# Kernel tuning notes

Hardware: AMD Instinct MI355X
Metric: run time of the kernel (lower is better)

## Reference

```python
import jax, jax.numpy as jnp
import numpy as np

EPS = 1e-5
_INV_STD = 1.0 / np.sqrt(1.0 + EPS)  # eval-mode BN with running_mean=0, running_var=1


def conv1x1(x, w):
    # x: (B,C,H,W), w: (O,C) -> (B,O,H,W)
    return jnp.einsum('bchw,oc->bohw', x, w)


def bn_relu(x, gamma, beta):
    y = x * (_INV_STD * gamma)[None, :, None, None] + beta[None, :, None, None]
    return jax.nn.relu(y)


def setup_inputs() -> dict:
    key = jax.random.key(0)
    ks = jax.random.split(key, 8)
    B, C, H, W, Kc, Kp = 8, 512, 128, 128, 256, 19
    s = 0.02
    return {
        'x': jax.random.normal(ks[0], (B, C, H, W), jnp.float32),
        'proxy_feats': jax.random.normal(ks[1], (B, C, Kp, 1), jnp.float32),
        'wq1': jax.random.normal(ks[2], (Kc, C), jnp.float32) * s,
        'gq1': jnp.ones((Kc,), jnp.float32), 'bq1': jnp.zeros((Kc,), jnp.float32),
        'wq2': jax.random.normal(ks[3], (Kc, Kc), jnp.float32) * s,
        'gq2': jnp.ones((Kc,), jnp.float32), 'bq2': jnp.zeros((Kc,), jnp.float32),
        'wk1': jax.random.normal(ks[4], (Kc, C), jnp.float32) * s,
        'gk1': jnp.ones((Kc,), jnp.float32), 'bk1': jnp.zeros((Kc,), jnp.float32),
        'wk2': jax.random.normal(ks[5], (Kc, Kc), jnp.float32) * s,
        'gk2': jnp.ones((Kc,), jnp.float32), 'bk2': jnp.zeros((Kc,), jnp.float32),
        'wv': jax.random.normal(ks[6], (Kc, C), jnp.float32) * s,
        'gv': jnp.ones((Kc,), jnp.float32), 'bv': jnp.zeros((Kc,), jnp.float32),
        'wo': jax.random.normal(ks[7], (C, Kc), jnp.float32) * s,
        'go': jnp.ones((C,), jnp.float32), 'bo': jnp.zeros((C,), jnp.float32),
    }


def reference(x, proxy_feats, wq1, gq1, bq1, wq2, gq2, bq2,
              wk1, gk1, bk1, wk2, gk2, bk2, wv, gv, bv, wo, go, bo):
    B, C, H, W = x.shape
    Kc = wq1.shape[0]
    # projections: 1x1 conv -> BN(eval) -> ReLU chains
    q = bn_relu(conv1x1(bn_relu(conv1x1(x, wq1), gq1, bq1), wq2), gq2, bq2)          # (B,Kc,H,W)
    k = bn_relu(conv1x1(bn_relu(conv1x1(proxy_feats, wk1), gk1, bk1), wk2), gk2, bk2)[..., 0]  # (B,Kc,Kp)
    v = bn_relu(conv1x1(proxy_feats, wv), gv, bv)[..., 0]                             # (B,Kc,Kp)
    qf = q.reshape(B, Kc, H * W).transpose(0, 2, 1)                                   # (B,HW,Kc)
    sim = jnp.einsum('bnc,bck->bnk', qf, k) * (Kc ** -0.5)                            # (B,HW,Kp)
    att = jax.nn.softmax(sim, axis=-1)
    ctx = jnp.einsum('bnk,bck->bnc', att, v)                                          # (B,HW,Kc)
    ctx = ctx.transpose(0, 2, 1).reshape(B, Kc, H, W)
    return bn_relu(conv1x1(ctx, wo), go, bo)                                          # (B,C,H,W)
```

## Files before the change

kernel.cpp:

```cpp
#include <hip/hip_runtime.h>

#define INV_STD 0.9999950000374997f

typedef unsigned short u16;
typedef __bf16 bf16x8 __attribute__((ext_vector_type(8)));
typedef __bf16 bf16x4 __attribute__((ext_vector_type(4)));
typedef float f32x4 __attribute__((ext_vector_type(4)));

__device__ __forceinline__ u16 f2bf(float f) {
    unsigned int u = __float_as_uint(f);
    u += 0x7fffu + ((u >> 16) & 1u);
    return (u16)(u >> 16);
}

__device__ __forceinline__ void gl_lds16(const void* g, void* l) {
    __builtin_amdgcn_global_load_lds(
        (const __attribute__((address_space(1))) unsigned int*)(unsigned long long)g,
        (__attribute__((address_space(3))) unsigned int*)(unsigned int)(unsigned long long)l,
        16, 0, 0);
}

__device__ __forceinline__ f32x4 mfma16(bf16x8 a, bf16x8 b, f32x4 c) {
    return __builtin_amdgcn_mfma_f32_16x16x32_bf16(a, b, c, 0, 0, 0);
}

__device__ __forceinline__ unsigned lds_off(const void* p) {
    return (unsigned)(unsigned long long)p;
}

__device__ __forceinline__ bf16x4 tr_read(unsigned addr) {
    bf16x4 r;
    asm volatile("ds_read_b64_tr_b16 %0, %1" : "=v"(r) : "v"(addr));
    return r;
}

__device__ __forceinline__ bf16x8 ldg8(const u16* p) {
    return *(const bf16x8*)p;
}

__global__ void wprep(const float* __restrict__ wq1, const float* __restrict__ gq1,
                      const float* __restrict__ wq2, const float* __restrict__ gq2,
                      u16* __restrict__ WQ1B, u16* __restrict__ WQ2B) {
    int blk = blockIdx.x;
    int t = threadIdx.x;
    if (blk < 512) {
        long i = (long)blk * 256 + t;
        int o = (int)(i >> 9);
        int q = (int)(i & 511);
        int r = q & 31;
        int src = (q & ~31) + ((r >> 3) & 3) * 4 + (r & 3) + ((r >> 2) & 1) * 16;
        WQ1B[i] = f2bf(wq1[(long)o * 512 + src] * (INV_STD * gq1[o]));
    } else {
        long i = (long)(blk - 512) * 256 + t;
        int o = (int)(i >> 8);
        WQ2B[i] = f2bf(wq2[i] * (INV_STD * gq2[o]));
    }
}

__global__ __launch_bounds__(256) void kv_kernel(
    const float* __restrict__ proxy,
    const float* __restrict__ wk1, const float* __restrict__ gk1, const float* __restrict__ bk1,
    const float* __restrict__ wk2, const float* __restrict__ gk2, const float* __restrict__ bk2,
    const float* __restrict__ wv,  const float* __restrict__ gv,  const float* __restrict__ bv,
    u16* __restrict__ KB,
    float* __restrict__ VF)
{
    int b = blockIdx.x >> 5, p = blockIdx.x & 31;
    int t = threadIdx.x;
    if (p >= 19) {
        KB[((long)b * 32 + p) * 256 + t] = 0;
        VF[((long)b * 256 + t) * 32 + p] = 0.f;
        return;
    }
    __shared__ float px[512];
    __shared__ float k1[256];
    for (int i = t; i < 512; i += 256) px[i] = proxy[((long)b * 512 + i) * 19 + p];
    __syncthreads();
    float aK = 0.f, aV = 0.f;
    const float4* wk1r = (const float4*)(wk1 + (long)t * 512);
    const float4* wvr  = (const float4*)(wv  + (long)t * 512);
    const float4* pxv  = (const float4*)px;
    #pragma unroll 4
    for (int c = 0; c < 128; ++c) {
        float4 pv = pxv[c];
        float4 k4 = wk1r[c];
        float4 v4 = wvr[c];
        aK += k4.x * pv.x + k4.y * pv.y + k4.z * pv.z + k4.w * pv.w;
        aV += v4.x * pv.x + v4.y * pv.y + v4.z * pv.z + v4.w * pv.w;
    }
    float k1v = fmaxf(aK * (INV_STD * gk1[t]) + bk1[t], 0.f);
    float vv  = fmaxf(aV * (INV_STD * gv[t])  + bv[t],  0.f);
    k1[t] = k1v;
    VF[((long)b * 256 + t) * 32 + p] = vv;
    __syncthreads();
    float a2 = 0.f;
    const float4* wk2r = (const float4*)(wk2 + (long)t * 256);
    const float4* k1v4 = (const float4*)k1;
    #pragma unroll 4
    for (int c = 0; c < 64; ++c) {
        float4 w4 = wk2r[c];
        float4 kk = k1v4[c];
        a2 += w4.x * kk.x + w4.y * kk.y + w4.z * kk.z + w4.w * kk.w;
    }
    KB[((long)b * 32 + p) * 256 + t] = f2bf(fmaxf(a2 * (INV_STD * gk2[t]) + bk2[t], 0.f));
}

__global__ __launch_bounds__(256) void wov_kernel(
    const float* __restrict__ wo,
    const float* __restrict__ go,
    const float* __restrict__ VF,
    u16* __restrict__ WoVB)
{
    int b = blockIdx.x >> 1, half = blockIdx.x & 1;
    __shared__ float vs[256 * 20];
    int t = threadIdx.x;
    #pragma unroll
    for (int p = 0; p < 19; ++p)
        vs[t * 20 + p] = VF[((long)b * 256 + t) * 32 + p];
    __syncthreads();
    int ch = half * 256 + t;
    float g = INV_STD * go[ch];
    const float* wr = wo + (long)ch * 256;
    float acc[19];
    #pragma unroll
    for (int p = 0; p < 19; ++p) acc[p] = 0.f;
    for (int c = 0; c < 256; ++c) {
        float wv = wr[c];
        #pragma unroll
        for (int p = 0; p < 19; ++p) acc[p] += wv * vs[c * 20 + p];
    }
    u16* dst = WoVB + ((long)b * 512 + ch) * 32;
    #pragma unroll
    for (int p = 0; p < 19; ++p) dst[p] = f2bf(g * acc[p]);
    #pragma unroll
    for (int p = 19; p < 32; ++p) dst[p] = 0;
}

__global__ __launch_bounds__(256, 2) void fused_all(
    const float* __restrict__ X,
    const u16* __restrict__ W1,
    const float* __restrict__ b1,
    const u16* __restrict__ W2,
    const float* __restrict__ b2,
    const u16* __restrict__ KB,
    const u16* __restrict__ WoVB,
    const float* __restrict__ obias,
    float* __restrict__ out)
{
    __shared__ __align__(16) u16 xs[64 * 64];
    __shared__ __align__(16) u16 lB[2][256 * 32];
    __shared__ __align__(16) u16 q12s[64 * 264];
    __shared__ __align__(16) u16 atts[64 * 40];
    int t = threadIdx.x, lane = t & 63, w = t >> 6;
    int l16 = lane & 15, hi = lane >> 4;
    long m0 = (long)blockIdx.x * 64;
    int b = (int)(m0 >> 14);
    int pixg = (int)(m0 & 16383);
    const float* xb = X + (long)b * 512 * 16384 + pixg;
    int ca = t >> 4;
    int aa = t & 15;
    int rW = lane >> 2;
    int cW = (lane & 3) << 3;
    unsigned trb = lds_off(&xs[hi * 64 + l16]);

    {
        f32x4 acc[4][4] = {};
        float4 xr0, xr1, xr2, xr3;
        {
            const float* p0 = xb + (long)ca * 16384 + aa * 4;
            xr0 = *(const float4*)(p0);
            xr1 = *(const float4*)(p0 + 16L * 16384);
            xr2 = *(const float4*)(p0 + 32L * 16384);
            xr3 = *(const float4*)(p0 + 48L * 16384);
        }
        #define STW(XR, P) { \
            int c = (P) * 16 + ca; \
            ushort4 u; u.x = f2bf(XR.x); u.y = f2bf(XR.y); u.z = f2bf(XR.z); u.w = f2bf(XR.w); \
            *(ushort4*)&xs[((aa >> 2) * 16 + (c >> 2)) * 64 + (c & 3) * 16 + (aa & 3) * 4] = u; }
        for (int kt = 0; kt < 8; ++kt) {
            int k0 = kt << 6;
            if (kt > 0) __syncthreads();
            STW(xr0, 0) STW(xr1, 1) STW(xr2, 2) STW(xr3, 3)
            __syncthreads();
            bf16x8 bb0[4], bb1[4];
            #pragma unroll
            for (int j = 0; j < 4; ++j) {
                const u16* wr = W1 + (long)(w * 64 + j * 16 + l16) * 512 + k0 + hi * 8;
                bb0[j] = ldg8(wr);
                bb1[j] = ldg8(wr + 32);
            }
            if (kt < 7) {
                const float* p0 = xb + (long)(k0 + 64 + ca) * 16384 + aa * 4;
                xr0 = *(const float4*)(p0);
                xr1 = *(const float4*)(p0 + 16L * 16384);
                xr2 = *(const float4*)(p0 + 32L * 16384);
                xr3 = *(const float4*)(p0 + 48L * 16384);
            }
            bf16x4 lo0[4], hh0[4], lo1[4], hh1[4];
            #pragma unroll
            for (int i = 0; i < 4; ++i) {
                unsigned a0 = trb + i * 2048;
                lo0[i] = tr_read(a0);
                hh0[i] = tr_read(a0 + 512);
            }
            #pragma unroll
            for (int i = 0; i < 4; ++i) {
                unsigned a0 = trb + i * 2048 + 1024;
                lo1[i] = tr_read(a0);
                hh1[i] = tr_read(a0 + 512);
            }
            asm volatile("s_waitcnt lgkmcnt(8)" ::: "memory");
            __builtin_amdgcn_sched_barrier(0);
            #pragma unroll
            for (int i = 0; i < 4; ++i) {
                bf16x8 a = __builtin_shufflevector(lo0[i], hh0[i], 0, 1, 2, 3, 4, 5, 6, 7);
                #pragma unroll
                for (int j = 0; j < 4; ++j)
                    acc[i][j] = mfma16(a, bb0[j], acc[i][j]);
            }
            asm volatile("s_waitcnt lgkmcnt(0)" ::: "memory");
            __builtin_amdgcn_sched_barrier(0);
            #pragma unroll
            for (int i = 0; i < 4; ++i) {
                bf16x8 a = __builtin_shufflevector(lo1[i], hh1[i], 0, 1, 2, 3, 4, 5, 6, 7);
                #pragma unroll
                for (int j = 0; j < 4; ++j)
                    acc[i][j] = mfma16(a, bb1[j], acc[i][j]);
            }
        }
        #undef STW
        #pragma unroll
        for (int j = 0; j < 4; ++j) {
            int q = w * 4 + j;
            gl_lds16(W2 + (long)(q * 16 + rW) * 256 + cW, &lB[0][q * 512]);
        }
        float bj[4];
        #pragma unroll
        for (int j = 0; j < 4; ++j) bj[j] = b1[w * 64 + j * 16 + l16];
        #pragma unroll
        for (int i = 0; i < 4; ++i)
            #pragma unroll
            for (int r = 0; r < 4; ++r) {
                int pix = i * 16 + hi * 4 + r;
                #pragma unroll
                for (int j = 0; j < 4; ++j) {
                    float v = acc[i][j][r] + bj[j];
                    q12s[pix * 264 + w * 64 + j * 16 + l16] = f2bf(fmaxf(v, 0.f));
                }
            }
    }
    __syncthreads();
    {
        f32x4 acc[4][4] = {};
        #pragma unroll
        for (int c = 0; c < 8; ++c) {
            int cur = c & 1;
            if (c < 7) {
                int k1 = (c + 1) << 5;
                #pragma unroll
                for (int j = 0; j < 4; ++j) {
                    int q = w * 4 + j;
                    gl_lds16(W2 + (long)(q * 16 + rW) * 256 + k1 + cW, &lB[cur ^ 1][q * 512]);
                }
            }
            bf16x8 a[4], bb[4];
            #pragma unroll
            for (int i = 0; i < 4; ++i)
                a[i] = *(const bf16x8*)&q12s[(i * 16 + l16) * 264 + (c << 5) + hi * 8];
            #pragma unroll
            for (int j = 0; j < 4; ++j)
                bb[j] = *(const bf16x8*)&lB[cur][(w * 64 + j * 16 + l16) * 32 + hi * 8];
            #pragma unroll
            for (int i = 0; i < 4; ++i)
                #pragma unroll
                for (int j = 0; j < 4; ++j)
                    acc[i][j] = mfma16(a[i], bb[j], acc[i][j]);
            __syncthreads();
        }
        float bj[4];
        #pragma unroll
        for (int j = 0; j < 4; ++j) bj[j] = b2[w * 64 + j * 16 + l16];
        #pragma unroll
        for (int i = 0; i < 4; ++i)
            #pragma unroll
            for (int r = 0; r < 4; ++r) {
                int pix = i * 16 + hi * 4 + r;
                #pragma unroll
                for (int j = 0; j < 4; ++j) {
                    float v = acc[i][j][r] + bj[j];
                    q12s[pix * 264 + w * 64 + j * 16 + l16] = f2bf(fmaxf(v, 0.f));
                }
            }
    }
    __syncthreads();
    {
        f32x4 s0 = {}, s1 = {};
        #pragma unroll
        for (int ks = 0; ks < 8; ++ks) {
            bf16x8 a = *(const bf16x8*)&q12s[(w * 16 + l16) * 264 + ks * 32 + hi * 8];
            bf16x8 b0 = ldg8(KB + ((long)b * 32 + l16) * 256 + ks * 32 + hi * 8);
            bf16x8 b1v = ldg8(KB + ((long)b * 32 + 16 + l16) * 256 + ks * 32 + hi * 8);
            s0 = mfma16(a, b0, s0);
            s1 = mfma16(a, b1v, s1);
        }
        const float scale = 0.0625f;
        #pragma unroll
        for (int r = 0; r < 4; ++r) {
            float v0 = s0[r] * scale;
            float v1 = s1[r] * scale;
            float mx = fmaxf(v0, v1);
            mx = fmaxf(mx, __shfl_xor(mx, 1));
            mx = fmaxf(mx, __shfl_xor(mx, 2));
            mx = fmaxf(mx, __shfl_xor(mx, 4));
            mx = fmaxf(mx, __shfl_xor(mx, 8));
            float e0 = __expf(v0 - mx);
            float e1 = (l16 < 3) ? __expf(v1 - mx) : 0.f;
            float s = e0 + e1;
            s += __shfl_xor(s, 1);
            s += __shfl_xor(s, 2);
            s += __shfl_xor(s, 4);
            s += __shfl_xor(s, 8);
            float inv = 1.f / s;
            int pix = w * 16 + hi * 4 + r;
            atts[pix * 40 + l16] = f2bf(e0 * inv);
            atts[pix * 40 + 16 + l16] = (l16 < 3) ? f2bf(e1 * inv) : (u16)0;
        }
    }
    __syncthreads();
    {
        bf16x8 av[4], bv[8];
        #pragma unroll
        for (int mf = 0; mf < 4; ++mf)
            av[mf] = *(const bf16x8*)&atts[(mf * 16 + l16) * 40 + hi * 8];
        #pragma unroll
        for (int nf = 0; nf < 8; ++nf)
            bv[nf] = ldg8(WoVB + ((long)b * 512 + w * 128 + nf * 16 + l16) * 32 + hi * 8);
        #pragma unroll
        for (int nf = 0; nf < 8; ++nf) {
            int ch = w * 128 + nf * 16 + l16;
            float bc = obias[ch];
            float* orow = out + ((long)b * 512 + ch) * 16384 + pixg;
            #pragma unroll
            for (int mf = 0; mf < 4; ++mf) {
                f32x4 acc = mfma16(av[mf], bv[nf], (f32x4){0.f, 0.f, 0.f, 0.f});
                float4 v;
                v.x = fmaxf(acc[0] + bc, 0.f);
                v.y = fmaxf(acc[1] + bc, 0.f);
                v.z = fmaxf(acc[2] + bc, 0.f);
                v.w = fmaxf(acc[3] + bc, 0.f);
                *(float4*)&orow[mf * 16 + hi * 4] = v;
            }
        }
    }
}

extern "C" void kernel_launch(void* const* d_in, const int* in_sizes, int n_in,
                              void* d_out, int out_size, void* d_ws, size_t ws_size,
                              hipStream_t stream) {
    const float* x    = (const float*)d_in[0];
    const float* prox = (const float*)d_in[1];
    const float* wq1  = (const float*)d_in[2];
    const float* gq1  = (const float*)d_in[3];
    const float* bq1  = (const float*)d_in[4];
    const float* wq2  = (const float*)d_in[5];
    const float* gq2  = (const float*)d_in[6];
    const float* bq2  = (const float*)d_in[7];
    const float* wk1  = (const float*)d_in[8];
    const float* gk1  = (const float*)d_in[9];
    const float* bk1  = (const float*)d_in[10];
    const float* wk2  = (const float*)d_in[11];
    const float* gk2  = (const float*)d_in[12];
    const float* bk2  = (const float*)d_in[13];
    const float* wv   = (const float*)d_in[14];
    const float* gv   = (const float*)d_in[15];
    const float* bv   = (const float*)d_in[16];
    const float* wo   = (const float*)d_in[17];
    const float* go   = (const float*)d_in[18];
    const float* bo   = (const float*)d_in[19];
    float* out = (float*)d_out;

    char* ws = (char*)d_ws;
    u16*   KB   = (u16*)(ws);
    float* VF   = (float*)(ws + 131072);
    u16*   WoVB = (u16*)(ws + 393216);
    u16*   WQ1B = (u16*)(ws + 655360);
    u16*   WQ2B = (u16*)(ws + 917504);

    wprep<<<768, 256, 0, stream>>>(wq1, gq1, wq2, gq2, WQ1B, WQ2B);
    kv_kernel<<<256, 256, 0, stream>>>(prox, wk1, gk1, bk1, wk2, gk2, bk2, wv, gv, bv, KB, VF);
    wov_kernel<<<16, 256, 0, stream>>>(wo, go, VF, WoVB);
    fused_all<<<2048, 256, 0, stream>>>(x, WQ1B, bq1, WQ2B, bq2, KB, WoVB, bo, out);
}
```

Measured before the change: 235.6 us.

## Load W2 fragments directly into registers instead of LDS double-buffering

The second GEMM (q1→q2) now loads its W2 B-operand fragments straight from global memory into registers, using a two-deep register prefetch with manual vmcnt waits, in place of the global_load_lds double buffer. This removes the 32KB lB LDS buffer and the per-iteration __syncthreads. With less LDS in use, launch bounds go from 2 to 3 blocks per SM for higher occupancy. The risks are register pressure under the tighter bound, which may cause spills, and exposed global-load latency, because W2 is now fetched per wave with no sharing through LDS.

Measured after the change: 268.7 us. 14.0% more time.

```diff
diff --git a/kernel.cpp b/kernel.cpp
--- a/kernel.cpp
+++ b/kernel.cpp
@@ -13,13 +13,6 @@
     return (u16)(u >> 16);
 }
 
-__device__ __forceinline__ void gl_lds16(const void* g, void* l) {
-    __builtin_amdgcn_global_load_lds(
-        (const __attribute__((address_space(1))) unsigned int*)(unsigned long long)g,
-        (__attribute__((address_space(3))) unsigned int*)(unsigned int)(unsigned long long)l,
-        16, 0, 0);
-}
-
 __device__ __forceinline__ f32x4 mfma16(bf16x8 a, bf16x8 b, f32x4 c) {
     return __builtin_amdgcn_mfma_f32_16x16x32_bf16(a, b, c, 0, 0, 0);
 }
@@ -36,6 +29,12 @@
 
 __device__ __forceinline__ bf16x8 ldg8(const u16* p) {
     return *(const bf16x8*)p;
+}
+
+__device__ __forceinline__ bf16x8 ldg8_asm(const u16* p) {
+    bf16x8 r;
+    asm volatile("global_load_dwordx4 %0, %1, off" : "=v"(r) : "v"(p));
+    return r;
 }
 
 __global__ void wprep(const float* __restrict__ wq1, const float* __restrict__ gq1,
@@ -136,7 +135,7 @@
     for (int p = 19; p < 32; ++p) dst[p] = 0;
 }
 
-__global__ __launch_bounds__(256, 2) void fused_all(
+__global__ __launch_bounds__(256, 3) void fused_all(
     const float* __restrict__ X,
     const u16* __restrict__ W1,
     const float* __restrict__ b1,
@@ -148,7 +147,6 @@
     float* __restrict__ out)
 {
     __shared__ __align__(16) u16 xs[64 * 64];
-    __shared__ __align__(16) u16 lB[2][256 * 32];
     __shared__ __align__(16) u16 q12s[64 * 264];
     __shared__ __align__(16) u16 atts[64 * 40];
     int t = threadIdx.x, lane = t & 63, w = t >> 6;
@@ -159,8 +157,6 @@
     const float* xb = X + (long)b * 512 * 16384 + pixg;
     int ca = t >> 4;
     int aa = t & 15;
-    int rW = lane >> 2;
-    int cW = (lane & 3) << 3;
     unsigned trb = lds_off(&xs[hi * 64 + l16]);
 
     {
@@ -229,11 +225,6 @@
             }
         }
         #undef STW
-        #pragma unroll
-        for (int j = 0; j < 4; ++j) {
-            int q = w * 4 + j;
-            gl_lds16(W2 + (long)(q * 16 + rW) * 256 + cW, &lB[0][q * 512]);
-        }
         float bj[4];
         #pragma unroll
         for (int j = 0; j < 4; ++j) bj[j] = b1[w * 64 + j * 16 + l16];
@@ -252,31 +243,52 @@
     __syncthreads();
     {
         f32x4 acc[4][4] = {};
+        const u16* wp0 = W2 + (long)(w * 64 +  0 + l16) * 256 + hi * 8;
+        const u16* wp1 = W2 + (long)(w * 64 + 16 + l16) * 256 + hi * 8;
+        const u16* wp2 = W2 + (long)(w * 64 + 32 + l16) * 256 + hi * 8;
+        const u16* wp3 = W2 + (long)(w * 64 + 48 + l16) * 256 + hi * 8;
+        bf16x8 wA0 = ldg8_asm(wp0),      wA1 = ldg8_asm(wp1),
+               wA2 = ldg8_asm(wp2),      wA3 = ldg8_asm(wp3);
+        bf16x8 wB0 = ldg8_asm(wp0 + 32), wB1 = ldg8_asm(wp1 + 32),
+               wB2 = ldg8_asm(wp2 + 32), wB3 = ldg8_asm(wp3 + 32);
         #pragma unroll
         for (int c = 0; c < 8; ++c) {
-            int cur = c & 1;
-            if (c < 7) {
-                int k1 = (c + 1) << 5;
-                #pragma unroll
-                for (int j = 0; j < 4; ++j) {
-                    int q = w * 4 + j;
-                    gl_lds16(W2 + (long)(q * 16 + rW) * 256 + k1 + cW, &lB[cur ^ 1][q * 512]);
-                }
-            }
-            bf16x8 a[4], bb[4];
+            bf16x8 a[4];
             #pragma unroll
             for (int i = 0; i < 4; ++i)
                 a[i] = *(const bf16x8*)&q12s[(i * 16 + l16) * 264 + (c << 5) + hi * 8];
-            #pragma unroll
-            for (int j = 0; j < 4; ++j)
-                bb[j] = *(const bf16x8*)&lB[cur][(w * 64 + j * 16 + l16) * 32 + hi * 8];
-            #pragma unroll
-            for (int i = 0; i < 4; ++i)
-                #pragma unroll
-                for (int j = 0; j < 4; ++j)
-                    acc[i][j] = mfma16(a[i], bb[j], acc[i][j]);
-            __syncthreads();
-        }
+            if (c < 7) asm volatile("s_waitcnt vmcnt(4)" ::: "memory");
+            else       asm volatile("s_waitcnt vmcnt(0)" ::: "memory");
+            __builtin_amdgcn_sched_barrier(0);
+            if ((c & 1) == 0) {
+                #pragma unroll
+                for (int i = 0; i < 4; ++i) {
+                    acc[i][0] = mfma16(a[i], wA0, acc[i][0]);
+                    acc[i][1] = mfma16(a[i], wA1, acc[i][1]);
+                    acc[i][2] = mfma16(a[i], wA2, acc[i][2]);
+                    acc[i][3] = mfma16(a[i], wA3, acc[i][3]);
+                }
+                if (c < 6) {
+                    int k2 = (c + 2) << 5;
+                    wA0 = ldg8_asm(wp0 + k2); wA1 = ldg8_asm(wp1 + k2);
+                    wA2 = ldg8_asm(wp2 + k2); wA3 = ldg8_asm(wp3 + k2);
+                }
+            } else {
+                #pragma unroll
+                for (int i = 0; i < 4; ++i) {
+                    acc[i][0] = mfma16(a[i], wB0, acc[i][0]);
+                    acc[i][1] = mfma16(a[i], wB1, acc[i][1]);
+                    acc[i][2] = mfma16(a[i], wB2, acc[i][2]);
+                    acc[i][3] = mfma16(a[i], wB3, acc[i][3]);
+                }
+                if (c < 6) {
+                    int k2 = (c + 2) << 5;
+                    wB0 = ldg8_asm(wp0 + k2); wB1 = ldg8_asm(wp1 + k2);
+                    wB2 = ldg8_asm(wp2 + k2); wB3 = ldg8_asm(wp3 + k2);
+                }
+            }
+        }
+        __syncthreads();
         float bj[4];
         #pragma unroll
         for (int j = 0; j < 4; ++j) bj[j] = b2[w * 64 + j * 16 + l16];
```
